# Performance work log

Measured on AMD Instinct MI355X. Metric: run time of the kernel, lower is better.

The kernel has to match this reference:

```python
import jax, jax.numpy as jnp
import numpy as np

B, N, H = 4, 4096, 64
T1 = 3072  # num_types = [0, 3072, 1024]


def _xavier(key, shape):
    fan_in, fan_out = shape[1], shape[0]
    lim = float(np.sqrt(6.0 / (fan_in + fan_out)))
    return jax.random.uniform(key, shape, jnp.float32, -lim, lim)


def setup_inputs() -> dict:
    key = jax.random.key(0)
    ks = jax.random.split(key, 16)
    adjacency = (jax.random.uniform(ks[0], (N, N)) < 0.05).astype(jnp.float32)
    adjacency = jnp.maximum(adjacency, jnp.eye(N, dtype=jnp.float32))  # avoid all-zero rows
    return {
        "hidden_states": jax.random.normal(ks[1], (B, N, H), jnp.float32),
        "input_states": jax.random.normal(ks[2], (B, 1, 1), jnp.float32),
        "adjacency": adjacency,
        "Wq": _xavier(ks[3], (H, H)),
        "Wk": _xavier(ks[4], (H, H)),
        "Wv": _xavier(ks[5], (H, H)),
        "Wu_inter": _xavier(ks[6], (H, H)),
        "bu_inter": jnp.zeros((H,), jnp.float32),
        "Wt_inter": _xavier(ks[7], (H, H)),
        "bt_inter": jnp.zeros((H,), jnp.float32),
        "Wu_out": _xavier(ks[8], (H, H)),
        "bu_out": jnp.zeros((H,), jnp.float32),
        "Wt_out": _xavier(ks[9], (H, H)),
        "bt_out": jnp.zeros((H,), jnp.float32),
        "step_size": jnp.float32(0.01),
    }


def reference(hidden_states, input_states, adjacency, Wq, Wk, Wv,
              Wu_inter, bu_inter, Wt_inter, bt_inter,
              Wu_out, bu_out, Wt_out, bt_out, step_size):
    # AccumulatorFunction: adjacency-masked QK^T, L2-norm rows (NOT softmax), aggregate V
    mask = adjacency.T  # [N, N]
    q = hidden_states @ Wq.T  # [B, N, H]
    k = hidden_states @ Wk.T
    v = hidden_states @ Wv.T
    rel = jnp.einsum('bnd,bmd->bnm', q, k) * mask  # [B, N, N]
    rel = rel / jnp.linalg.norm(rel, axis=2, keepdims=True)
    acc = jnp.einsum('bnm,bmd->bnd', rel, v)  # [B, N, H]

    # update_hidden_states with num_types = [0, T1, N - T1]
    def branch(h, a, Wu, bu, Wt, bt):
        dt = 2.0 * jax.nn.sigmoid(h @ Wt.T + bt) - 1.0
        return h + step_size * dt * (a @ Wu.T + bu)

    upd_inter = branch(hidden_states[:, :T1], acc[:, :T1],
                       Wu_inter, bu_inter, Wt_inter, bt_inter)
    upd_out = branch(hidden_states[:, T1:], acc[:, T1:],
                     Wu_out, bu_out, Wt_out, bt_out)
    return jnp.concatenate([upd_inter, upd_out], axis=1)  # [B, N, H]
```

## Files before the change

kernel.cpp:

```cpp
#include <hip/hip_runtime.h>
#include <hip/hip_bf16.h>
#include <math.h>

#define Bb 4
#define Nn 4096
#define Hh 64
#define T1c 3072
#define MC 4

typedef unsigned short ushort_t;
typedef __bf16 bf16x8 __attribute__((ext_vector_type(8)));
typedef float floatx4 __attribute__((ext_vector_type(4)));
typedef unsigned short ushort4v __attribute__((ext_vector_type(4)));

__device__ ushort_t g_qw[(size_t)Bb * Nn * Hh];
__device__ ushort_t g_kw[(size_t)Bb * Nn * Hh];
__device__ ushort_t g_vt[(size_t)Bb * Nn * Hh];
__device__ ushort_t g_dt[(size_t)Bb * Nn * Hh];
__device__ float    g_pac[(size_t)Bb * 64 * MC * 64 * 64];
__device__ float    g_pss[(size_t)Bb * 64 * MC * 64];

__device__ __forceinline__ float bf2f(unsigned short u) {
    union { unsigned int i; float f; } c;
    c.i = ((unsigned int)u) << 16;
    return c.f;
}
__device__ __forceinline__ unsigned short f2bf(float f) {
    union { float f; unsigned int i; } c;
    c.f = f;
    unsigned int x = c.i;
    unsigned int r = (x + 0x7fffu + ((x >> 16) & 1u)) >> 16;
    return (unsigned short)r;
}

__device__ __forceinline__ bf16x8 ld8(const void* p, size_t eidx, bool f32) {
    if (f32) {
        const float* fp = (const float*)p + eidx;
        float4 x0 = *(const float4*)fp;
        float4 x1 = *(const float4*)(fp + 4);
        bf16x8 r;
        r[0] = (__bf16)x0.x; r[1] = (__bf16)x0.y; r[2] = (__bf16)x0.z; r[3] = (__bf16)x0.w;
        r[4] = (__bf16)x1.x; r[5] = (__bf16)x1.y; r[6] = (__bf16)x1.z; r[7] = (__bf16)x1.w;
        return r;
    }
    return *(const bf16x8*)((const ushort_t*)p + eidx);
}
__device__ __forceinline__ float ldS(const void* p, size_t eidx, bool f32) {
    return f32 ? ((const float*)p)[eidx] : bf2f(((const ushort_t*)p)[eidx]);
}
__device__ __forceinline__ void stOut(void* p, size_t eidx, float v, bool f32) {
    if (f32) ((float*)p)[eidx] = v;
    else ((ushort_t*)p)[eidx] = f2bf(v);
}

__device__ __forceinline__ floatx4 mfma16(bf16x8 a, bf16x8 b, floatx4 c) {
    return __builtin_amdgcn_mfma_f32_16x16x32_bf16(a, b, c, 0, 0, 0);
}

__device__ __forceinline__ float fast_tanh(float x) {
    float e = __expf(-2.0f * fabsf(x));
    float t = (1.0f - e) / (1.0f + e);
    return copysignf(t, x);
}

__global__ __launch_bounds__(256) void qkvt_kernel(
    const void* __restrict__ hid, const void* __restrict__ adj,
    const void* __restrict__ Wq, const void* __restrict__ Wk,
    const void* __restrict__ Wv,
    const void* __restrict__ Wti, const void* __restrict__ bti,
    const void* __restrict__ Wto, const void* __restrict__ bto)
{
    const bool F32 = (*(const unsigned*)adj) == 0x3F800000u;

    const int bi = blockIdx.x;
    const int b = bi >> 8;
    const int n16 = (bi & 255) << 4;
    const int t = threadIdx.x;
    const int wv = t >> 6, lane = t & 63, l16 = lane & 15, quad = lane >> 4;
    const bool inter = (n16 < T1c);

    const void* W = (wv == 0) ? Wq : (wv == 1) ? Wk : (wv == 2) ? Wv
                    : (inter ? Wti : Wto);
    const void* bt = inter ? bti : bto;

    const size_t hbase = ((size_t)(b * Nn + n16 + l16)) * Hh + quad * 8;
    bf16x8 a0 = ld8(hid, hbase, F32);
    bf16x8 a1 = ld8(hid, hbase + 32, F32);
    floatx4 z = {0.f, 0.f, 0.f, 0.f};

    floatx4 c[4];
#pragma unroll
    for (int ti = 0; ti < 4; ++ti) {
        const size_t wrow = (size_t)(ti * 16 + l16) * 64 + quad * 8;
        bf16x8 w0 = ld8(W, wrow, F32);
        bf16x8 w1 = ld8(W, wrow + 32, F32);
        c[ti] = mfma16(a1, w1, mfma16(a0, w0, z));
    }

    if (wv == 0 || wv == 1) {
        ushort_t* dst = (wv == 0) ? g_qw : g_kw;
#pragma unroll
        for (int ti = 0; ti < 4; ++ti)
#pragma unroll
            for (int r = 0; r < 4; ++r)
                dst[((size_t)(b * Nn + n16 + quad * 4 + r)) * 64 + ti * 16 + l16] = f2bf(c[ti][r]);
    } else if (wv == 2) {
#pragma unroll
        for (int ti = 0; ti < 4; ++ti) {
            uint2 pk;
            pk.x = (unsigned)f2bf(c[ti][0]) | ((unsigned)f2bf(c[ti][1]) << 16);
            pk.y = (unsigned)f2bf(c[ti][2]) | ((unsigned)f2bf(c[ti][3]) << 16);
            *(uint2*)&g_vt[((size_t)(b * 64 + ti * 16 + l16)) * Nn + n16 + quad * 4] = pk;
        }
    } else {
#pragma unroll
        for (int ti = 0; ti < 4; ++ti) {
            const float btv = ldS(bt, ti * 16 + l16, F32);
#pragma unroll
            for (int r = 0; r < 4; ++r)
                g_dt[((size_t)(b * Nn + n16 + quad * 4 + r)) * 64 + ti * 16 + l16] =
                    f2bf(fast_tanh(0.5f * (c[ti][r] + btv)));
        }
    }
}

__global__ __launch_bounds__(256) void attn_part_kernel(
    const void* __restrict__ adj)
{
    const bool F32 = (*(const unsigned*)adj) == 0x3F800000u;

    __shared__ ushort_t adjT[64 * 72];
    __shared__ ushort_t kT[64 * 72];
    __shared__ ushort_t vTl[64 * 72];
    __shared__ ushort_t sS[64 * 72];

    const int bi = blockIdx.x;
    const int b = bi & 3;
    const int mc = (bi >> 2) & 3;
    const int nt = bi >> 4;
    const int n0 = nt << 6;
    const int t = threadIdx.x;
    const int wv = t >> 6, lane = t & 63, l16 = lane & 15, quad = lane >> 4;
    const int nw = n0 + wv * 16;
    const int nnb = wv * 16 + quad * 4;

    const size_t qbase = ((size_t)(b * Nn + nw + l16)) * 64 + quad * 8;
    bf16x8 a0 = *(const bf16x8*)&g_qw[qbase];
    bf16x8 a1 = *(const bf16x8*)&g_qw[qbase + 32];

    floatx4 z = {0.f, 0.f, 0.f, 0.f};
    floatx4 acc[4];
    float ssq[4];
#pragma unroll
    for (int i = 0; i < 4; ++i) { acc[i] = z; ssq[i] = 0.f; }

    int srow[2], scol[2];
#pragma unroll
    for (int i = 0; i < 2; ++i) { const int cc = t + 256 * i; srow[i] = cc >> 3; scol[i] = (cc & 7) * 8; }

    for (int it = 0; it < 1024 / 64; ++it) {
        const int m0 = mc * 1024 + it * 64;

#pragma unroll
        for (int i = 0; i < 2; ++i) {
            *(bf16x8*)&adjT[srow[i] * 72 + scol[i]] =
                ld8(adj, (size_t)(m0 + srow[i]) * Nn + n0 + scol[i], F32);
            *(bf16x8*)&kT[srow[i] * 72 + scol[i]] =
                *(const bf16x8*)&g_kw[((size_t)(b * Nn + m0 + srow[i])) * 64 + scol[i]];
            *(bf16x8*)&vTl[srow[i] * 72 + scol[i]] =
                *(const bf16x8*)&g_vt[((size_t)(b * 64 + srow[i])) * Nn + m0 + scol[i]];
        }
        __syncthreads();

#pragma unroll
        for (int tm = 0; tm < 4; ++tm) {
            const ushort_t* kb = &kT[(tm * 16 + l16) * 72];
            bf16x8 k0 = *(const bf16x8*)(kb + quad * 8);
            bf16x8 k1 = *(const bf16x8*)(kb + 32 + quad * 8);
            floatx4 sv = mfma16(a1, k1, mfma16(a0, k0, z));
            ushort4v mv = *(const ushort4v*)&adjT[(tm * 16 + l16) * 72 + nnb];
#pragma unroll
            for (int r = 0; r < 4; ++r) {
                const float sm = sv[r] * bf2f(mv[r]);
                ssq[r] += sm * sm;
                sS[(nnb + r) * 72 + tm * 16 + l16] = f2bf(sm);
            }
        }
        __syncthreads();

        bf16x8 sa0 = *(const bf16x8*)&sS[(wv * 16 + l16) * 72 + quad * 8];
        bf16x8 sa1 = *(const bf16x8*)&sS[(wv * 16 + l16) * 72 + 32 + quad * 8];
#pragma unroll
        for (int td = 0; td < 4; ++td) {
            const ushort_t* vb = &vTl[(td * 16 + l16) * 72];
            bf16x8 v0 = *(const bf16x8*)(vb + quad * 8);
            bf16x8 v1 = *(const bf16x8*)(vb + 32 + quad * 8);
            acc[td] = mfma16(sa0, v0, acc[td]);
            acc[td] = mfma16(sa1, v1, acc[td]);
        }
        __syncthreads();
    }

#pragma unroll
    for (int r = 0; r < 4; ++r) {
        float v = ssq[r];
        v += __shfl_xor(v, 1, 64);
        v += __shfl_xor(v, 2, 64);
        v += __shfl_xor(v, 4, 64);
        v += __shfl_xor(v, 8, 64);
        ssq[r] = v;
    }
    const size_t pbase = ((size_t)(b * 64 + nt) * MC + mc);
    if (l16 == 0) {
#pragma unroll
        for (int r = 0; r < 4; ++r)
            g_pss[pbase * 64 + nnb + r] = ssq[r];
    }
#pragma unroll
    for (int td = 0; td < 4; ++td)
#pragma unroll
        for (int r = 0; r < 4; ++r)
            g_pac[(pbase * 64 + nnb + r) * 64 + td * 16 + l16] = acc[td][r];
}

__global__ __launch_bounds__(256) void finish_kernel(
    const void* __restrict__ hid, const void* __restrict__ adj,
    const void* __restrict__ Wui, const void* __restrict__ bui,
    const void* __restrict__ Wuo, const void* __restrict__ buo,
    const void* __restrict__ stepp, void* __restrict__ outp)
{
    const bool F32 = (*(const unsigned*)adj) == 0x3F800000u;

    const int bi = blockIdx.x;
    const int b = bi >> 8;
    const int r16 = bi & 255;
    const int n16 = r16 << 4;
    const int nt = r16 >> 2;
    const int nloc0 = (r16 & 3) << 4;
    const int t = threadIdx.x;
    const int wv = t >> 6, lane = t & 63, l16 = lane & 15, quad = lane >> 4;

    const size_t sbase = ((size_t)(b * 64 + nt) * MC + quad) * 64 + nloc0 + l16;
    float sv = g_pss[sbase];
    sv += __shfl_xor(sv, 16, 64);
    sv += __shfl_xor(sv, 32, 64);
    const float inv = (sv > 0.f) ? __frsqrt_rn(sv) : 0.f;

    float s0[8], s1[8];
#pragma unroll
    for (int j = 0; j < 8; ++j) { s0[j] = 0.f; s1[j] = 0.f; }
#pragma unroll
    for (int mcq = 0; mcq < MC; ++mcq) {
        const size_t abase =
            (((size_t)(b * 64 + nt) * MC + mcq) * 64 + nloc0 + l16) * 64 + quad * 8;
        float4 x0 = *(const float4*)&g_pac[abase];
        float4 x1 = *(const float4*)&g_pac[abase + 4];
        float4 y0 = *(const float4*)&g_pac[abase + 32];
        float4 y1 = *(const float4*)&g_pac[abase + 36];
        s0[0] += x0.x; s0[1] += x0.y; s0[2] += x0.z; s0[3] += x0.w;
        s0[4] += x1.x; s0[5] += x1.y; s0[6] += x1.z; s0[7] += x1.w;
        s1[0] += y0.x; s1[1] += y0.y; s1[2] += y0.z; s1[3] += y0.w;
        s1[4] += y1.x; s1[5] += y1.y; s1[6] += y1.z; s1[7] += y1.w;
    }
    bf16x8 ua0, ua1;
#pragma unroll
    for (int j = 0; j < 8; ++j) {
        ua0[j] = (__bf16)(s0[j] * inv);
        ua1[j] = (__bf16)(s1[j] * inv);
    }

    const bool inter = (n16 < T1c);
    const void* Wu = inter ? Wui : Wuo;
    const void* bu = inter ? bui : buo;
    const float step = ldS(stepp, 0, F32);

    const int ti = wv;
    floatx4 z = {0.f, 0.f, 0.f, 0.f};
    const size_t wrow = (size_t)(ti * 16 + l16) * 64 + quad * 8;
    bf16x8 w0 = ld8(Wu, wrow, F32);
    bf16x8 w1 = ld8(Wu, wrow + 32, F32);
    floatx4 u = mfma16(ua1, w1, mfma16(ua0, w0, z));
    const float buv = ldS(bu, ti * 16 + l16, F32);
#pragma unroll
    for (int r = 0; r < 4; ++r) {
        const size_t idx = ((size_t)(b * Nn + n16 + quad * 4 + r)) * 64 + ti * 16 + l16;
        const float hv = ldS(hid, idx, F32);
        const float dtv = bf2f(g_dt[idx]);
        stOut(outp, idx, hv + step * dtv * (u[r] + buv), F32);
    }
}

extern "C" void kernel_launch(void* const* d_in, const int* in_sizes, int n_in,
                              void* d_out, int out_size, void* d_ws, size_t ws_size,
                              hipStream_t stream)
{
    const void* hid = d_in[0];
    const void* adj = d_in[2];
    const void* Wq  = d_in[3];
    const void* Wk  = d_in[4];
    const void* Wv  = d_in[5];
    const void* Wui = d_in[6];
    const void* bui = d_in[7];
    const void* Wti = d_in[8];
    const void* bti = d_in[9];
    const void* Wuo = d_in[10];
    const void* buo = d_in[11];
    const void* Wto = d_in[12];
    const void* bto = d_in[13];
    const void* stepp = d_in[14];

    qkvt_kernel<<<dim3(Bb * (Nn / 16)), dim3(256), 0, stream>>>(
        hid, adj, Wq, Wk, Wv, Wti, bti, Wto, bto);
    attn_part_kernel<<<dim3(Bb * 64 * MC), dim3(256), 0, stream>>>(adj);
    finish_kernel<<<dim3(Bb * (Nn / 16)), dim3(256), 0, stream>>>(
        hid, adj, Wui, bui, Wuo, buo, stepp, d_out);
}
```

Baseline: 200.5 us.

## Use 32x32 MFMA tiles and bitmask adjacency in attention partial kernel

Rewrites the attention partial kernel so each wave computes a 32x32 tile with the 32x32x16 bf16 MFMA instead of 16x16 tiles. The adjacency tile is packed into a per-row bitmask in shared memory instead of being stored as bf16, and the block-index mapping is reordered so batch is the outer dimension. Partial sums of squares are now reduced across waves through shared memory with an extra barrier. The intent is fewer MFMA and LDS instructions and less shared-memory traffic, at the cost of more registers per thread and extra bit-packing work during loads.

Result: faster. 182.3 us (-9.1%).

```diff
diff --git a/kernel.cpp b/kernel.cpp
--- a/kernel.cpp
+++ b/kernel.cpp
@@ -11,6 +11,7 @@
 typedef unsigned short ushort_t;
 typedef __bf16 bf16x8 __attribute__((ext_vector_type(8)));
 typedef float floatx4 __attribute__((ext_vector_type(4)));
+typedef float floatx16 __attribute__((ext_vector_type(16)));
 typedef unsigned short ushort4v __attribute__((ext_vector_type(4)));
 
 __device__ ushort_t g_qw[(size_t)Bb * Nn * Hh];
@@ -56,6 +57,9 @@
 __device__ __forceinline__ floatx4 mfma16(bf16x8 a, bf16x8 b, floatx4 c) {
     return __builtin_amdgcn_mfma_f32_16x16x32_bf16(a, b, c, 0, 0, 0);
 }
+__device__ __forceinline__ floatx16 mfma32(bf16x8 a, bf16x8 b, floatx16 c) {
+    return __builtin_amdgcn_mfma_f32_32x32x16_bf16(a, b, c, 0, 0, 0);
+}
 
 __device__ __forceinline__ float fast_tanh(float x) {
     float e = __expf(-2.0f * fabsf(x));
@@ -124,35 +128,36 @@
     }
 }
 
-__global__ __launch_bounds__(256) void attn_part_kernel(
+__global__ __launch_bounds__(256, 4) void attn_part_kernel(
     const void* __restrict__ adj)
 {
     const bool F32 = (*(const unsigned*)adj) == 0x3F800000u;
 
-    __shared__ ushort_t adjT[64 * 72];
-    __shared__ ushort_t kT[64 * 72];
-    __shared__ ushort_t vTl[64 * 72];
-    __shared__ ushort_t sS[64 * 72];
+    __shared__ __align__(16) ushort_t kT[64 * 72];
+    __shared__ __align__(16) ushort_t vTl[64 * 72];
+    __shared__ __align__(16) ushort_t sS[64 * 72];
+    __shared__ __align__(4)  unsigned char bmB[64 * 8];
+    __shared__ float ssqArr[4 * 64];
 
     const int bi = blockIdx.x;
-    const int b = bi & 3;
-    const int mc = (bi >> 2) & 3;
-    const int nt = bi >> 4;
+    const int b  = bi >> 8;
+    const int mc = bi & 3;
+    const int nt = (bi >> 2) & 63;
     const int n0 = nt << 6;
     const int t = threadIdx.x;
-    const int wv = t >> 6, lane = t & 63, l16 = lane & 15, quad = lane >> 4;
-    const int nw = n0 + wv * 16;
-    const int nnb = wv * 16 + quad * 4;
-
-    const size_t qbase = ((size_t)(b * Nn + nw + l16)) * 64 + quad * 8;
-    bf16x8 a0 = *(const bf16x8*)&g_qw[qbase];
-    bf16x8 a1 = *(const bf16x8*)&g_qw[qbase + 32];
-
-    floatx4 z = {0.f, 0.f, 0.f, 0.f};
-    floatx4 acc[4];
-    float ssq[4];
-#pragma unroll
-    for (int i = 0; i < 4; ++i) { acc[i] = z; ssq[i] = 0.f; }
+    const int wv = t >> 6, lane = t & 63;
+    const int l32 = lane & 31, h = lane >> 5;
+    const int nh = wv >> 1, mh = wv & 1;
+
+    bf16x8 qf[4];
+#pragma unroll
+    for (int i = 0; i < 4; ++i)
+        qf[i] = *(const bf16x8*)&g_qw[((size_t)(b * Nn + n0 + nh * 32 + l32)) * 64 + h * 8 + 16 * i];
+
+    floatx16 acc;
+    float ssq[16];
+#pragma unroll
+    for (int r = 0; r < 16; ++r) { acc[r] = 0.f; ssq[r] = 0.f; }
 
     int srow[2], scol[2];
 #pragma unroll
@@ -163,64 +168,86 @@
 
 #pragma unroll
         for (int i = 0; i < 2; ++i) {
-            *(bf16x8*)&adjT[srow[i] * 72 + scol[i]] =
-                ld8(adj, (size_t)(m0 + srow[i]) * Nn + n0 + scol[i], F32);
             *(bf16x8*)&kT[srow[i] * 72 + scol[i]] =
                 *(const bf16x8*)&g_kw[((size_t)(b * Nn + m0 + srow[i])) * 64 + scol[i]];
             *(bf16x8*)&vTl[srow[i] * 72 + scol[i]] =
                 *(const bf16x8*)&g_vt[((size_t)(b * 64 + srow[i])) * Nn + m0 + scol[i]];
+            unsigned byte = 0;
+            if (F32) {
+                const float* fp = (const float*)adj + (size_t)(m0 + srow[i]) * Nn + n0 + scol[i];
+                float4 x0 = *(const float4*)fp;
+                float4 x1 = *(const float4*)(fp + 4);
+                byte = (unsigned)(x0.x != 0.f)        | ((unsigned)(x0.y != 0.f) << 1)
+                     | ((unsigned)(x0.z != 0.f) << 2) | ((unsigned)(x0.w != 0.f) << 3)
+                     | ((unsigned)(x1.x != 0.f) << 4) | ((unsigned)(x1.y != 0.f) << 5)
+                     | ((unsigned)(x1.z != 0.f) << 6) | ((unsigned)(x1.w != 0.f) << 7);
+            } else {
+                const ushort_t* up = (const ushort_t*)adj + (size_t)(m0 + srow[i]) * Nn + n0 + scol[i];
+#pragma unroll
+                for (int j = 0; j < 8; ++j) byte |= (unsigned)(up[j] != 0) << j;
+            }
+            bmB[srow[i] * 8 + (scol[i] >> 3)] = (unsigned char)byte;
         }
         __syncthreads();
 
-#pragma unroll
-        for (int tm = 0; tm < 4; ++tm) {
-            const ushort_t* kb = &kT[(tm * 16 + l16) * 72];
-            bf16x8 k0 = *(const bf16x8*)(kb + quad * 8);
-            bf16x8 k1 = *(const bf16x8*)(kb + 32 + quad * 8);
-            floatx4 sv = mfma16(a1, k1, mfma16(a0, k0, z));
-            ushort4v mv = *(const ushort4v*)&adjT[(tm * 16 + l16) * 72 + nnb];
-#pragma unroll
-            for (int r = 0; r < 4; ++r) {
-                const float sm = sv[r] * bf2f(mv[r]);
-                ssq[r] += sm * sm;
-                sS[(nnb + r) * 72 + tm * 16 + l16] = f2bf(sm);
-            }
+        floatx16 s;
+#pragma unroll
+        for (int r = 0; r < 16; ++r) s[r] = 0.f;
+#pragma unroll
+        for (int i = 0; i < 4; ++i) {
+            bf16x8 kf = *(const bf16x8*)&kT[(mh * 32 + l32) * 72 + h * 8 + 16 * i];
+            s = mfma32(qf[i], kf, s);
+        }
+        const unsigned mw = *(const unsigned*)&bmB[(mh * 32 + l32) * 8 + nh * 4];
+        __bf16* sSb = (__bf16*)sS;
+#pragma unroll
+        for (int r = 0; r < 16; ++r) {
+            const int rp = (r & 3) + 8 * (r >> 2) + 4 * h;
+            const float sm = ((mw >> rp) & 1u) ? s[r] : 0.f;
+            ssq[r] += sm * sm;
+            sSb[(nh * 32 + rp) * 72 + mh * 32 + l32] = (__bf16)sm;
         }
         __syncthreads();
 
-        bf16x8 sa0 = *(const bf16x8*)&sS[(wv * 16 + l16) * 72 + quad * 8];
-        bf16x8 sa1 = *(const bf16x8*)&sS[(wv * 16 + l16) * 72 + 32 + quad * 8];
-#pragma unroll
-        for (int td = 0; td < 4; ++td) {
-            const ushort_t* vb = &vTl[(td * 16 + l16) * 72];
-            bf16x8 v0 = *(const bf16x8*)(vb + quad * 8);
-            bf16x8 v1 = *(const bf16x8*)(vb + 32 + quad * 8);
-            acc[td] = mfma16(sa0, v0, acc[td]);
-            acc[td] = mfma16(sa1, v1, acc[td]);
+#pragma unroll
+        for (int i = 0; i < 4; ++i) {
+            bf16x8 sf = *(const bf16x8*)&sS[(nh * 32 + l32) * 72 + h * 8 + 16 * i];
+            bf16x8 vf = *(const bf16x8*)&vTl[(mh * 32 + l32) * 72 + h * 8 + 16 * i];
+            acc = mfma32(sf, vf, acc);
         }
         __syncthreads();
     }
 
-#pragma unroll
-    for (int r = 0; r < 4; ++r) {
+    const size_t pbase = ((size_t)(b * 64 + nt) * MC + mc);
+
+#pragma unroll
+    for (int r = 0; r < 16; ++r) {
         float v = ssq[r];
         v += __shfl_xor(v, 1, 64);
         v += __shfl_xor(v, 2, 64);
         v += __shfl_xor(v, 4, 64);
         v += __shfl_xor(v, 8, 64);
+        v += __shfl_xor(v, 16, 64);
         ssq[r] = v;
     }
-    const size_t pbase = ((size_t)(b * 64 + nt) * MC + mc);
-    if (l16 == 0) {
-#pragma unroll
-        for (int r = 0; r < 4; ++r)
-            g_pss[pbase * 64 + nnb + r] = ssq[r];
-    }
-#pragma unroll
-    for (int td = 0; td < 4; ++td)
-#pragma unroll
-        for (int r = 0; r < 4; ++r)
-            g_pac[(pbase * 64 + nnb + r) * 64 + td * 16 + l16] = acc[td][r];
+    if (l32 == 0) {
+#pragma unroll
+        for (int r = 0; r < 16; ++r) {
+            const int rp = (r & 3) + 8 * (r >> 2) + 4 * h;
+            ssqArr[wv * 64 + nh * 32 + rp] = ssq[r];
+        }
+    }
+    __syncthreads();
+    if (t < 64) {
+        const int w0 = (t >> 5) * 2;
+        g_pss[pbase * 64 + t] = ssqArr[w0 * 64 + t] + ssqArr[(w0 + 1) * 64 + t];
+    }
+
+#pragma unroll
+    for (int r = 0; r < 16; ++r) {
+        const int n = nh * 32 + (r & 3) + 8 * (r >> 2) + 4 * h;
+        g_pac[(pbase * 64 + n) * 64 + mh * 32 + l32] = acc[r];
+    }
 }
 
 __global__ __launch_bounds__(256) void finish_kernel(
```
